# Kernel tuning notes

Measured on AMD Instinct MI355X. Metric: run time of the kernel, lower is better.

The kernel has to match this reference:

```python
import jax, jax.numpy as jnp
import numpy as np

N = 50000        # nodes
E = 800000       # edges
F_IN = 16        # num_features
F_EDGE = 8       # num_edge_features
H = 4            # heads
C = 32           # hidden_dim (per-head out channels)
D = H * C        # 128, node state width
NUM_CLASSES = 5
NEG_SLOPE = 0.2  # PyG GATConv default leaky_relu slope


def setup_inputs() -> dict:
    key = jax.random.key(0)
    ks = jax.random.split(key, 30)
    def w(k, shape):
        return jax.random.normal(k, shape, dtype=jnp.float32) * 0.05
    return {
        "x": jax.random.normal(ks[0], (N, F_IN), dtype=jnp.float32),
        "edge_index": jax.random.randint(ks[1], (2, E), 0, N),
        "edge_attr": jax.random.normal(ks[2], (E, F_EDGE), dtype=jnp.float32),
        # edge_encoder: Linear(F_EDGE->C), ReLU, Linear(C->H)
        "ee_w1": w(ks[3], (C, F_EDGE)), "ee_b1": jnp.zeros((C,), jnp.float32),
        "ee_w2": w(ks[4], (H, C)),      "ee_b2": jnp.zeros((H,), jnp.float32),
        # input_proj: Linear(F_IN -> D)
        "proj_w": w(ks[5], (D, F_IN)), "proj_b": jnp.zeros((D,), jnp.float32),
        # conv1: GATConv(F_IN, C, heads=H, edge_dim=H, concat=True)
        "c1_lin": w(ks[6], (D, F_IN)),
        "c1_att_src": w(ks[7], (H, C)), "c1_att_dst": w(ks[8], (H, C)),
        "c1_lin_edge": w(ks[9], (D, H)), "c1_att_edge": w(ks[10], (H, C)),
        "c1_bias": jnp.zeros((D,), jnp.float32),
        # conv2: GATConv(D, C, heads=H, edge_dim=H, concat=True)
        "c2_lin": w(ks[11], (D, D)),
        "c2_att_src": w(ks[12], (H, C)), "c2_att_dst": w(ks[13], (H, C)),
        "c2_lin_edge": w(ks[14], (D, H)), "c2_att_edge": w(ks[15], (H, C)),
        "c2_bias": jnp.zeros((D,), jnp.float32),
        # layer norms
        "n1_g": jnp.ones((D,), jnp.float32), "n1_b": jnp.zeros((D,), jnp.float32),
        "n2_g": jnp.ones((D,), jnp.float32), "n2_b": jnp.zeros((D,), jnp.float32),
        # jk_proj: Linear(3D -> D)
        "jk_w": w(ks[16], (D, 3 * D)), "jk_b": jnp.zeros((D,), jnp.float32),
        # classifier: Linear(D -> NUM_CLASSES)
        "cls_w": w(ks[17], (NUM_CLASSES, D)), "cls_b": jnp.zeros((NUM_CLASSES,), jnp.float32),
    }


def _layer_norm(h, g, b, eps=1e-5):
    mu = jnp.mean(h, axis=-1, keepdims=True)
    var = jnp.var(h, axis=-1, keepdims=True)
    return (h - mu) * jax.lax.rsqrt(var + eps) * g + b


def _gat_conv(x, src, dst, e_attr, lin_w, att_src, att_dst, lin_edge_w, att_edge, bias):
    """PyG GATConv (v1) with edge features, concat=True, eval mode (no dropout)."""
    n = x.shape[0]
    xs = (x @ lin_w.T).reshape(n, H, C)                      # [N,H,C]
    a_src = jnp.einsum('nhc,hc->nh', xs, att_src)            # [N,H]
    a_dst = jnp.einsum('nhc,hc->nh', xs, att_dst)            # [N,H]
    ee = (e_attr @ lin_edge_w.T).reshape(-1, H, C)           # [E,H,C]
    a_edge = jnp.einsum('ehc,hc->eh', ee, att_edge)          # [E,H]
    alpha = jax.nn.leaky_relu(a_src[src] + a_dst[dst] + a_edge, NEG_SLOPE)
    # segment softmax over destination neighborhoods
    amax = jax.ops.segment_max(alpha, dst, num_segments=n)
    ex = jnp.exp(alpha - amax[dst])
    denom = jax.ops.segment_sum(ex, dst, num_segments=n)
    alpha = ex / (denom[dst] + 1e-16)                        # [E,H]
    msg = xs[src] * alpha[:, :, None]                        # [E,H,C]
    out = jax.ops.segment_sum(msg, dst, num_segments=n)      # [N,H,C]
    return out.reshape(n, H * C) + bias


def reference(x, edge_index, edge_attr,
              ee_w1, ee_b1, ee_w2, ee_b2,
              proj_w, proj_b,
              c1_lin, c1_att_src, c1_att_dst, c1_lin_edge, c1_att_edge, c1_bias,
              c2_lin, c2_att_src, c2_att_dst, c2_lin_edge, c2_att_edge, c2_bias,
              n1_g, n1_b, n2_g, n2_b,
              jk_w, jk_b, cls_w, cls_b):
    src, dst = edge_index[0], edge_index[1]
    # edge encoder
    e = jax.nn.relu(edge_attr @ ee_w1.T + ee_b1) @ ee_w2.T + ee_b2   # [E,H]
    h0 = x @ proj_w.T + proj_b                                        # [N,D]
    h1 = _gat_conv(x, src, dst, e, c1_lin, c1_att_src, c1_att_dst,
                   c1_lin_edge, c1_att_edge, c1_bias)
    h1 = _layer_norm(jax.nn.elu(h1) + h0, n1_g, n1_b)
    h2 = _gat_conv(h1, src, dst, e, c2_lin, c2_att_src, c2_att_dst,
                   c2_lin_edge, c2_att_edge, c2_bias)
    h2 = _layer_norm(jax.nn.elu(h2) + h1, n2_g, n2_b)
    h = jnp.concatenate([h0, h1, h2], axis=-1) @ jk_w.T + jk_b
    out = h @ cls_w.T + cls_b
    return jax.nn.log_softmax(out, axis=1)
```

## Files before the change

kernel.cpp:

```cpp
#include <hip/hip_runtime.h>
#include <cstdint>

#define NN 50000
#define NE 800000
#define DPX 6250
#define SLICES 391

using short8  = __attribute__((ext_vector_type(8))) short;
using float4v = __attribute__((ext_vector_type(4))) float;
using floatx2 = __attribute__((ext_vector_type(2))) float;
typedef unsigned char uchar;

__device__ __forceinline__ ushort f2bf(float f) {
    uint u = __float_as_uint(f);
    uint r = (u + 0x7fffu + ((u >> 16) & 1u)) >> 16;
    return (ushort)r;
}
__device__ __forceinline__ float bf2f(uint u) {
    return __uint_as_float(u << 16);
}
__device__ __forceinline__ uchar f2fp8(float v) {
    return (uchar)((uint)__builtin_amdgcn_cvt_pk_fp8_f32(v, v, 0, false) & 0xffu);
}

__global__ __launch_bounds__(256) void k_prep2(const float* __restrict__ le1, const float* __restrict__ ae1,
                                               const float* __restrict__ le2, const float* __restrict__ ae2,
                                               const float* __restrict__ jkw, const float* __restrict__ jkb,
                                               const float* __restrict__ clw, const float* __restrict__ clb,
                                               const float* __restrict__ projw, const float* __restrict__ c1lin,
                                               const float* __restrict__ c2lin,
                                               const float* __restrict__ asrc1, const float* __restrict__ adst1,
                                               float* __restrict__ M, float* __restrict__ CW,
                                               float* __restrict__ cbp,
                                               ushort* __restrict__ w01b, ushort* __restrict__ c2b,
                                               float* __restrict__ Vmat, int* __restrict__ deg)
{
    int idx = blockIdx.x * 256 + threadIdx.x;
    if (idx < NN) deg[idx] = 0;
    if (idx < 32) {
        const float* le = (idx < 16) ? le1 : le2;
        const float* ae = (idx < 16) ? ae1 : ae2;
        int hk = idx & 15, h = hk >> 2, k = hk & 3;
        float s = 0.f;
        for (int c = 0; c < 32; ++c)
            s += le[(h * 32 + c) * 4 + k] * ae[h * 32 + c];
        M[idx] = s;
    } else if (idx < 1952) {
        int o = idx - 32;
        int r = o / 384, c = o - r * 384;
        float s = 0.f;
        for (int k = 0; k < 128; ++k)
            s += clw[r * 128 + k] * jkw[(size_t)k * 384 + c];
        CW[o] = s;
    } else if (idx < 1957) {
        int r = idx - 1952;
        float s = clb[r];
        for (int k = 0; k < 128; ++k)
            s += clw[r * 128 + k] * jkb[k];
        cbp[r] = s;
    } else if (idx >= 2048 && idx < 10240) {
        int o = idx - 2048;
        int r = o >> 5, c = o & 31;
        float v = 0.f;
        if (c < 16) v = (r < 128) ? projw[r * 16 + c] : c1lin[(r - 128) * 16 + c];
        w01b[o] = f2bf(v);
    } else if (idx >= 10240 && idx < 26624) {
        int o = idx - 10240;
        c2b[o] = f2bf(c2lin[o]);
    } else if (idx >= 26624 && idx < 26752) {
        int o = idx - 26624;
        const float* att = (o < 64) ? asrc1 : adst1;
        int oo = o & 63, h = oo >> 4, k = oo & 15;
        float s = 0.f;
        for (int c = 0; c < 32; ++c)
            s += c1lin[(h * 32 + c) * 16 + k] * att[h * 32 + c];
        Vmat[o] = s;
    }
}

__global__ __launch_bounds__(256) void k_att1(const float* __restrict__ x,
                                              const float* __restrict__ V,
                                              float* __restrict__ as_o,
                                              float* __restrict__ ad_o)
{
    __shared__ float sV[128];
    int t = threadIdx.x;
    if (t < 128) sV[t] = V[t];
    __syncthreads();
    int n = blockIdx.x * 256 + t;
    if (n >= NN) return;
    const float4* xr = (const float4*)(x + (size_t)n * 16);
    float4 x0 = xr[0], x1 = xr[1], x2 = xr[2], x3 = xr[3];
    float xv[16] = {x0.x,x0.y,x0.z,x0.w, x1.x,x1.y,x1.z,x1.w,
                    x2.x,x2.y,x2.z,x2.w, x3.x,x3.y,x3.z,x3.w};
    float s[4], d[4];
    #pragma unroll
    for (int h = 0; h < 4; ++h) {
        float ss = 0.f, dd = 0.f;
        #pragma unroll
        for (int k = 0; k < 16; ++k) {
            ss += xv[k] * sV[h * 16 + k];
            dd += xv[k] * sV[64 + h * 16 + k];
        }
        s[h] = ss; d[h] = dd;
    }
    *(float4*)(as_o + (size_t)n * 4) = make_float4(s[0], s[1], s[2], s[3]);
    *(float4*)(ad_o + (size_t)n * 4) = make_float4(d[0], d[1], d[2], d[3]);
}

__global__ __launch_bounds__(256) void k_edge_mlp(const float* __restrict__ ea,
                                                  const float* __restrict__ w1,
                                                  const float* __restrict__ b1,
                                                  const float* __restrict__ w2,
                                                  const float* __restrict__ b2,
                                                  const int* __restrict__ ei,
                                                  const float* __restrict__ Mm,
                                                  const float* __restrict__ as1,
                                                  const float* __restrict__ ad1,
                                                  ushort* __restrict__ exb,
                                                  uint* __restrict__ aeq)
{
    __shared__ float sw1[256], sb1[32], sw2[128], sb2[4], sM[32];
    int t = threadIdx.x;
    sw1[t] = w1[t];
    if (t < 128) sw2[t] = w2[t];
    if (t < 32)  { sb1[t] = b1[t]; sM[t] = Mm[t]; }
    if (t < 4)   sb2[t] = b2[t];
    __syncthreads();
    int e = blockIdx.x * 256 + t;
    if (e >= NE) return;
    int src = ei[e], dst = ei[NE + e];
    float4 s4 = *(const float4*)(as1 + (size_t)src * 4);
    float4 d4 = *(const float4*)(ad1 + (size_t)dst * 4);
    float4 x0 = *(const float4*)(ea + (size_t)e * 8);
    float4 x1 = *(const float4*)(ea + (size_t)e * 8 + 4);
    float o0 = sb2[0], o1 = sb2[1], o2 = sb2[2], o3 = sb2[3];
    #pragma unroll
    for (int j = 0; j < 32; ++j) {
        const float* w = sw1 + j * 8;
        float s = sb1[j] + w[0]*x0.x + w[1]*x0.y + w[2]*x0.z + w[3]*x0.w
                         + w[4]*x1.x + w[5]*x1.y + w[6]*x1.z + w[7]*x1.w;
        s = fmaxf(s, 0.f);
        o0 += sw2[0*32+j] * s; o1 += sw2[1*32+j] * s;
        o2 += sw2[2*32+j] * s; o3 += sw2[3*32+j] * s;
    }
    float sa[4] = {s4.x, s4.y, s4.z, s4.w};
    float da[4] = {d4.x, d4.y, d4.z, d4.w};
    ushort exq[4];
    float a2[4];
    #pragma unroll
    for (int h = 0; h < 4; ++h) {
        float ae1 = sM[h*4+0]*o0 + sM[h*4+1]*o1 + sM[h*4+2]*o2 + sM[h*4+3]*o3;
        float al = sa[h] + da[h] + ae1;
        al = al > 0.f ? al : 0.2f * al;
        exq[h] = f2bf(__expf(al));
        a2[h] = sM[16+h*4+0]*o0 + sM[16+h*4+1]*o1 + sM[16+h*4+2]*o2 + sM[16+h*4+3]*o3;
    }
    *(uint2*)(exb + (size_t)e * 4) =
        make_uint2((uint)exq[0] | ((uint)exq[1] << 16), (uint)exq[2] | ((uint)exq[3] << 16));
    uint q = (uint)__builtin_amdgcn_cvt_pk_fp8_f32(a2[0], a2[1], 0, false);
    q = (uint)__builtin_amdgcn_cvt_pk_fp8_f32(a2[2], a2[3], (int)q, true);
    aeq[e] = q;
}

__global__ __launch_bounds__(256) void k_hist8(const int* __restrict__ ei, int* __restrict__ deg)
{
    int grp = blockIdx.x & 7;
    int base = (blockIdx.x >> 3) * 2048 + threadIdx.x;
    #pragma unroll
    for (int k = 0; k < 8; ++k) {
        int e = base + k * 256;
        if (e < NE) {
            int dst = ei[NE + e];
            if (dst / DPX == grp) atomicAdd(&deg[dst], 1);
        }
    }
}

__global__ __launch_bounds__(256) void k_scan_blk(const int* __restrict__ deg,
                                                  int* __restrict__ loc,
                                                  int* __restrict__ bsum)
{
    __shared__ int tmp[256];
    int t = threadIdx.x;
    int i = blockIdx.x * 256 + t;
    int v = (i < NN) ? deg[i] : 0;
    tmp[t] = v;
    __syncthreads();
    #pragma unroll
    for (int o = 1; o < 256; o <<= 1) {
        int add = (t >= o) ? tmp[t - o] : 0;
        __syncthreads();
        tmp[t] += add;
        __syncthreads();
    }
    if (i < NN) loc[i] = tmp[t] - v;
    if (t == 255) bsum[blockIdx.x] = tmp[255];
}

__global__ __launch_bounds__(256) void k_scan_top(const int* __restrict__ bsum,
                                                  int* __restrict__ bcarry,
                                                  int* __restrict__ total_out, int nb)
{
    __shared__ int tmp[256];
    int t = threadIdx.x;
    int v = (t < nb) ? bsum[t] : 0;
    tmp[t] = v;
    __syncthreads();
    #pragma unroll
    for (int o = 1; o < 256; o <<= 1) {
        int add = (t >= o) ? tmp[t - o] : 0;
        __syncthreads();
        tmp[t] += add;
        __syncthreads();
    }
    if (t < nb) bcarry[t] = tmp[t] - v;
    if (t == 255) *total_out = tmp[255];
}

__global__ __launch_bounds__(256) void k_scan_add(const int* __restrict__ loc,
                                                  const int* __restrict__ bcarry,
                                                  int* __restrict__ off,
                                                  int* __restrict__ cur)
{
    int i = blockIdx.x * 256 + threadIdx.x;
    if (i < NN) {
        int o = loc[i] + bcarry[blockIdx.x];
        off[i] = o;
        cur[i] = o;
    }
}

__global__ __launch_bounds__(256) void k_scatter8(const int* __restrict__ ei,
                                                  const ushort* __restrict__ exb,
                                                  const uint* __restrict__ aeq,
                                                  int* __restrict__ cursor,
                                                  int4* __restrict__ csr4)
{
    int grp = blockIdx.x & 7;
    int base = (blockIdx.x >> 3) * 2048 + threadIdx.x;
    #pragma unroll
    for (int k = 0; k < 8; ++k) {
        int e = base + k * 256;
        if (e < NE) {
            int dst = ei[NE + e];
            if (dst / DPX == grp) {
                int src = ei[e];
                uint2 ex = *(const uint2*)(exb + (size_t)e * 4);
                uint q = aeq[e];
                int p = atomicAdd(&cursor[dst], 1);
                csr4[p] = make_int4((src << 16) | dst, (int)ex.x, (int)ex.y, (int)q);
            }
        }
    }
}

__global__ __launch_bounds__(256) void k_gemm1(const float* __restrict__ x,
                                               const ushort* __restrict__ w01,
                                               const float* __restrict__ pbias,
                                               ushort* __restrict__ hcatb,
                                               uchar* __restrict__ xs8, int M)
{
    int t = threadIdx.x;
    int wv = t >> 6, lane = t & 63;
    int quad = lane >> 4, r16 = lane & 15;
    int m0 = blockIdx.x * 128 + wv * 32;
    int ar0 = m0 + r16;      if (ar0 >= M) ar0 = M - 1;
    int ar1 = m0 + 16 + r16; if (ar1 >= M) ar1 = M - 1;
    short8 a0 = (short8){0,0,0,0,0,0,0,0}, a1 = a0;
    if (quad < 2) {
        const float* p0 = x + (size_t)ar0 * 16 + quad * 8;
        const float* p1 = x + (size_t)ar1 * 16 + quad * 8;
        float4 u0 = *(const float4*)p0, u1 = *(const float4*)(p0 + 4);
        float4 v0 = *(const float4*)p1, v1 = *(const float4*)(p1 + 4);
        a0[0]=(short)f2bf(u0.x); a0[1]=(short)f2bf(u0.y); a0[2]=(short)f2bf(u0.z); a0[3]=(short)f2bf(u0.w);
        a0[4]=(short)f2bf(u1.x); a0[5]=(short)f2bf(u1.y); a0[6]=(short)f2bf(u1.z); a0[7]=(short)f2bf(u1.w);
        a1[0]=(short)f2bf(v0.x); a1[1]=(short)f2bf(v0.y); a1[2]=(short)f2bf(v0.z); a1[3]=(short)f2bf(v0.w);
        a1[4]=(short)f2bf(v1.x); a1[5]=(short)f2bf(v1.y); a1[6]=(short)f2bf(v1.z); a1[7]=(short)f2bf(v1.w);
    }
    float4v acc[2][16];
    #pragma unroll
    for (int i = 0; i < 2; ++i)
        #pragma unroll
        for (int j = 0; j < 16; ++j) acc[i][j] = (float4v){0.f, 0.f, 0.f, 0.f};
    #pragma unroll
    for (int nt = 0; nt < 16; ++nt) {
        short8 b = *(const short8*)(w01 + (size_t)(nt * 16 + r16) * 32 + quad * 8);
        acc[0][nt] = __builtin_amdgcn_mfma_f32_16x16x32_bf16(a0, b, acc[0][nt], 0, 0, 0);
        acc[1][nt] = __builtin_amdgcn_mfma_f32_16x16x32_bf16(a1, b, acc[1][nt], 0, 0, 0);
    }
    #pragma unroll
    for (int rt = 0; rt < 2; ++rt) {
        #pragma unroll
        for (int nt = 0; nt < 16; ++nt) {
            int col = (nt & 7) * 16 + r16;
            float bv = (nt < 8) ? pbias[col] : 0.f;
            #pragma unroll
            for (int r = 0; r < 4; ++r) {
                int row = m0 + rt * 16 + quad * 4 + r;
                if (row < M) {
                    float v = acc[rt][nt][r] + bv;
                    if (nt < 8) hcatb[(size_t)row * 384 + col] = f2bf(v);
                    else        xs8[(size_t)row * 128 + col] = f2fp8(v);
                }
            }
        }
    }
}

__global__ __launch_bounds__(256) void k_gemm2(const ushort* __restrict__ A,
                                               const ushort* __restrict__ W,
                                               const float* __restrict__ atts,
                                               const float* __restrict__ attd,
                                               uchar* __restrict__ xs8,
                                               float* __restrict__ as_o,
                                               float* __restrict__ ad_o, int M)
{
    __shared__ float sAs[128], sAd[128];
    int t = threadIdx.x;
    if (t < 128) { sAs[t] = atts[t]; sAd[t] = attd[t]; }
    __syncthreads();
    int wv = t >> 6, lane = t & 63;
    int quad = lane >> 4, r16 = lane & 15;
    int m0 = blockIdx.x * 128 + wv * 32;
    float4v acc[2][8];
    #pragma unroll
    for (int i = 0; i < 2; ++i)
        #pragma unroll
        for (int j = 0; j < 8; ++j) acc[i][j] = (float4v){0.f, 0.f, 0.f, 0.f};
    int ar0 = m0 + r16;      if (ar0 >= M) ar0 = M - 1;
    int ar1 = m0 + 16 + r16; if (ar1 >= M) ar1 = M - 1;
    const ushort* a0p = A + (size_t)ar0 * 384 + quad * 8;
    const ushort* a1p = A + (size_t)ar1 * 384 + quad * 8;
    const ushort* wp  = W + (size_t)r16 * 128 + quad * 8;
    #pragma unroll
    for (int k0 = 0; k0 < 128; k0 += 32) {
        short8 a0 = *(const short8*)(a0p + k0);
        short8 a1 = *(const short8*)(a1p + k0);
        #pragma unroll
        for (int nt = 0; nt < 8; ++nt) {
            short8 b = *(const short8*)(wp + (size_t)(nt * 16) * 128 + k0);
            acc[0][nt] = __builtin_amdgcn_mfma_f32_16x16x32_bf16(a0, b, acc[0][nt], 0, 0, 0);
            acc[1][nt] = __builtin_amdgcn_mfma_f32_16x16x32_bf16(a1, b, acc[1][nt], 0, 0, 0);
        }
    }
    #pragma unroll
    for (int rt = 0; rt < 2; ++rt) {
        #pragma unroll
        for (int nt = 0; nt < 8; ++nt) {
            int col = nt * 16 + r16;
            #pragma unroll
            for (int r = 0; r < 4; ++r) {
                int row = m0 + rt * 16 + quad * 4 + r;
                if (row < M)
                    xs8[(size_t)row * 128 + col] = f2fp8(acc[rt][nt][r]);
            }
        }
        #pragma unroll
        for (int r = 0; r < 4; ++r) {
            int row = m0 + rt * 16 + quad * 4 + r;
            float sh[4], dh[4];
            #pragma unroll
            for (int h = 0; h < 4; ++h) {
                int cA = h * 32 + r16, cB = cA + 16;
                sh[h] = acc[rt][2*h][r] * sAs[cA] + acc[rt][2*h+1][r] * sAs[cB];
                dh[h] = acc[rt][2*h][r] * sAd[cA] + acc[rt][2*h+1][r] * sAd[cB];
            }
            #pragma unroll
            for (int o = 1; o < 16; o <<= 1) {
                #pragma unroll
                for (int h = 0; h < 4; ++h) {
                    sh[h] += __shfl_xor(sh[h], o, 64);
                    dh[h] += __shfl_xor(dh[h], o, 64);
                }
            }
            if (r16 == 0 && row < M) {
                *(float4*)(as_o + (size_t)row * 4) = make_float4(sh[0], sh[1], sh[2], sh[3]);
                *(float4*)(ad_o + (size_t)row * 4) = make_float4(dh[0], dh[1], dh[2], dh[3]);
            }
        }
    }
}

__global__ __launch_bounds__(256) void k_soft2csr(int4* __restrict__ csr4,
                                                  const float* __restrict__ as_in,
                                                  const float* __restrict__ ad_in)
{
    int i = blockIdx.x * 256 + threadIdx.x;
    if (i >= NE) return;
    int4 en = csr4[i];
    uint sd = (uint)en.x;
    int src = (int)(sd >> 16), dst = (int)(sd & 0xffffu);
    float4 s4 = *(const float4*)(as_in + (size_t)src * 4);
    float4 d4 = *(const float4*)(ad_in + (size_t)dst * 4);
    floatx2 a01 = __builtin_amdgcn_cvt_pk_f32_fp8(en.w, false);
    floatx2 a23 = __builtin_amdgcn_cvt_pk_f32_fp8(en.w, true);
    float av[4] = {a01.x, a01.y, a23.x, a23.y};
    float sa[4] = {s4.x, s4.y, s4.z, s4.w};
    float da[4] = {d4.x, d4.y, d4.z, d4.w};
    ushort exq[4];
    #pragma unroll
    for (int h = 0; h < 4; ++h) {
        float al = sa[h] + da[h] + av[h];
        al = al > 0.f ? al : 0.2f * al;
        exq[h] = f2bf(__expf(al));
    }
    en.y = (int)((uint)exq[0] | ((uint)exq[1] << 16));
    en.z = (int)((uint)exq[2] | ((uint)exq[3] << 16));
    csr4[i] = en;
}

__global__ __launch_bounds__(256) void k_agg2(const int* __restrict__ off,
                                              const int4* __restrict__ csr4,
                                              const uchar* __restrict__ xs8,
                                              const float* __restrict__ bias,
                                              const ushort* __restrict__ residb,
                                              const float* __restrict__ g,
                                              const float* __restrict__ bln,
                                              ushort* __restrict__ outb)
{
    int wave = threadIdx.x >> 6;
    int lane = threadIdx.x & 63;
    int n = blockIdx.x * 4 + wave;
    if (n >= NN) return;
    int i0 = off[n], i1 = off[n + 1];
    int c0 = lane * 2;
    int h = lane >> 4;
    int hsel = h >> 1, hsh = (h & 1) << 4;
    float a0 = 0.f, a1 = 0.f, den = 0.f;
    int i = i0;
    for (; i + 8 <= i1; i += 8) {
        int4 en[8];
        #pragma unroll
        for (int j = 0; j < 8; ++j) en[j] = csr4[i + j];
        ushort p[8];
        #pragma unroll
        for (int j = 0; j < 8; ++j)
            p[j] = *(const ushort*)(xs8 + (size_t)((uint)en[j].x >> 16) * 128 + c0);
        #pragma unroll
        for (int j = 0; j < 8; ++j) {
            uint exsel = (uint)(hsel ? en[j].z : en[j].y);
            float w = bf2f((exsel >> hsh) & 0xffffu);
            floatx2 v = __builtin_amdgcn_cvt_pk_f32_fp8((int)(uint)p[j], false);
            a0 = fmaf(v.x, w, a0);
            a1 = fmaf(v.y, w, a1);
            den += w;
        }
    }
    for (; i + 4 <= i1; i += 4) {
        int4 en[4];
        #pragma unroll
        for (int j = 0; j < 4; ++j) en[j] = csr4[i + j];
        ushort p[4];
        #pragma unroll
        for (int j = 0; j < 4; ++j)
            p[j] = *(const ushort*)(xs8 + (size_t)((uint)en[j].x >> 16) * 128 + c0);
        #pragma unroll
        for (int j = 0; j < 4; ++j) {
            uint exsel = (uint)(hsel ? en[j].z : en[j].y);
            float w = bf2f((exsel >> hsh) & 0xffffu);
            floatx2 v = __builtin_amdgcn_cvt_pk_f32_fp8((int)(uint)p[j], false);
            a0 = fmaf(v.x, w, a0);
            a1 = fmaf(v.y, w, a1);
            den += w;
        }
    }
    for (; i < i1; ++i) {
        int4 en = csr4[i];
        ushort p0 = *(const ushort*)(xs8 + (size_t)((uint)en.x >> 16) * 128 + c0);
        uint exsel = (uint)(hsel ? en.z : en.y);
        float w = bf2f((exsel >> hsh) & 0xffffu);
        floatx2 v = __builtin_amdgcn_cvt_pk_f32_fp8((int)(uint)p0, false);
        a0 = fmaf(v.x, w, a0);
        a1 = fmaf(v.y, w, a1);
        den += w;
    }
    float inv = 1.f / (den + 1e-16f);
    float v0 = a0 * inv + bias[c0];
    float v1 = a1 * inv + bias[c0 + 1];
    v0 = v0 > 0.f ? v0 : (__expf(v0) - 1.f);
    v1 = v1 > 0.f ? v1 : (__expf(v1) - 1.f);
    uint rp = *(const uint*)(residb + (size_t)n * 384 + c0);
    float r0 = v0 + bf2f(rp & 0xffffu);
    float r1 = v1 + bf2f(rp >> 16);
    float ssum = r0 + r1, ssq = r0 * r0 + r1 * r1;
    #pragma unroll
    for (int o = 1; o < 64; o <<= 1) {
        ssum += __shfl_xor(ssum, o, 64);
        ssq  += __shfl_xor(ssq, o, 64);
    }
    float mu = ssum * (1.f / 128.f);
    float var = ssq * (1.f / 128.f) - mu * mu;
    float rs = rsqrtf(var + 1e-5f);
    float o0 = (r0 - mu) * rs * g[c0] + bln[c0];
    float o1 = (r1 - mu) * rs * g[c0 + 1] + bln[c0 + 1];
    uint pk = (uint)f2bf(o0) | ((uint)f2bf(o1) << 16);
    *(uint*)(outb + (size_t)n * 384 + c0) = pk;
}

__global__ __launch_bounds__(256) void k_cls(const ushort* __restrict__ hcatb,
                                             const float* __restrict__ CW,
                                             const float* __restrict__ cbp,
                                             float* __restrict__ out)
{
    __shared__ float sCW[1920], scb[5];
    int t = threadIdx.x;
    for (int i = t; i < 1920; i += 256) sCW[i] = CW[i];
    if (t < 5) scb[t] = cbp[t];
    __syncthreads();
    int n = blockIdx.x * 256 + t;
    if (n >= NN) return;
    float acc[5] = {scb[0], scb[1], scb[2], scb[3], scb[4]};
    const uint2* hr = (const uint2*)(hcatb + (size_t)n * 384);
    #pragma unroll 4
    for (int q = 0; q < 96; ++q) {
        uint2 p = hr[q];
        float v0 = bf2f(p.x & 0xffffu), v1 = bf2f(p.x >> 16);
        float v2 = bf2f(p.y & 0xffffu), v3 = bf2f(p.y >> 16);
        #pragma unroll
        for (int o = 0; o < 5; ++o) {
            const float* w = sCW + o * 384 + q * 4;
            acc[o] += v0*w[0] + v1*w[1] + v2*w[2] + v3*w[3];
        }
    }
    float m = acc[0];
    #pragma unroll
    for (int o = 1; o < 5; ++o) m = fmaxf(m, acc[o]);
    float sum = 0.f;
    #pragma unroll
    for (int o = 0; o < 5; ++o) sum += __expf(acc[o] - m);
    float lse = __logf(sum) + m;
    float* op = out + (size_t)n * 5;
    #pragma unroll
    for (int o = 0; o < 5; ++o) op[o] = acc[o] - lse;
}

extern "C" void kernel_launch(void* const* d_in, const int* in_sizes, int n_in,
                              void* d_out, int out_size, void* d_ws, size_t ws_size,
                              hipStream_t stream)
{
    (void)in_sizes; (void)n_in; (void)out_size; (void)ws_size;
    const float* x        = (const float*)d_in[0];
    const int*   ei       = (const int*)d_in[1];
    const float* eattr    = (const float*)d_in[2];
    const float* ee_w1    = (const float*)d_in[3];
    const float* ee_b1    = (const float*)d_in[4];
    const float* ee_w2    = (const float*)d_in[5];
    const float* ee_b2    = (const float*)d_in[6];
    const float* proj_w   = (const float*)d_in[7];
    const float* proj_b   = (const float*)d_in[8];
    const float* c1_lin   = (const float*)d_in[9];
    const float* c1_asrc  = (const float*)d_in[10];
    const float* c1_adst  = (const float*)d_in[11];
    const float* c1_ledge = (const float*)d_in[12];
    const float* c1_aedge = (const float*)d_in[13];
    const float* c1_bias  = (const float*)d_in[14];
    const float* c2_lin   = (const float*)d_in[15];
    const float* c2_asrc  = (const float*)d_in[16];
    const float* c2_adst  = (const float*)d_in[17];
    const float* c2_ledge = (const float*)d_in[18];
    const float* c2_aedge = (const float*)d_in[19];
    const float* c2_bias  = (const float*)d_in[20];
    const float* n1_g     = (const float*)d_in[21];
    const float* n1_b     = (const float*)d_in[22];
    const float* n2_g     = (const float*)d_in[23];
    const float* n2_b     = (const float*)d_in[24];
    const float* jk_w     = (const float*)d_in[25];
    const float* jk_b     = (const float*)d_in[26];
    const float* cls_w    = (const float*)d_in[27];
    const float* cls_b    = (const float*)d_in[28];
    float* out = (float*)d_out;
    float* ws  = (float*)d_ws;

    const size_t oM   = 0;
    const size_t oCW  = 64;
    const size_t oCB  = 1984;
    const size_t oV   = 2048;
    const size_t oEX  = 2176;
    const size_t oAQ  = oEX + (size_t)NE * 2;
    const size_t oHB  = oAQ + (size_t)NE;
    const size_t oXS  = oHB + (size_t)NN * 192;
    const size_t oWB  = oXS + (size_t)NN * 32;
    const size_t oAS  = oWB + 12288;
    const size_t oAD  = oAS + (size_t)NN * 4;
    const size_t oI   = oAD + (size_t)NN * 4;

    float*  Mmat  = ws + oM;
    float*  CW    = ws + oCW;
    float*  cbp   = ws + oCB;
    float*  Vmat  = ws + oV;
    ushort* exb   = (ushort*)(ws + oEX);
    uint*   aeq   = (uint*)(ws + oAQ);
    ushort* hcatb = (ushort*)(ws + oHB);
    uchar*  xs8   = (uchar*)(ws + oXS);
    ushort* w01b  = (ushort*)(ws + oWB);
    ushort* c2b   = w01b + 8192;
    float*  as_b  = ws + oAS;
    float*  ad_b  = ws + oAD;
    int*    ip    = (int*)(ws + oI);
    int*    deg   = ip;
    int*    loc   = ip + NN;
    int*    off   = ip + 2 * NN;
    int*    cur   = ip + 3 * NN + 16;
    int*    bsum  = ip + 4 * NN + 16;
    int*    bcar  = ip + 4 * NN + 272;
    int4*   csr4  = (int4*)(ip + 4 * NN + 544);

    const int EB  = (NE + 255) / 256;
    const int NB  = (NN + 255) / 256;
    const int GB  = (NN + 127) / 128;
    const int WB2 = (NN + 3) / 4;
    const int PB  = SLICES * 8;

    k_prep2<<<NB, 256, 0, stream>>>(c1_ledge, c1_aedge, c2_ledge, c2_aedge,
                                    jk_w, jk_b, cls_w, cls_b,
                                    proj_w, c1_lin, c2_lin, c1_asrc, c1_adst,
                                    Mmat, CW, cbp, w01b, c2b, Vmat, deg);
    k_att1<<<NB, 256, 0, stream>>>(x, Vmat, as_b, ad_b);
    k_edge_mlp<<<EB, 256, 0, stream>>>(eattr, ee_w1, ee_b1, ee_w2, ee_b2, ei,
                                       Mmat, as_b, ad_b, exb, aeq);
    k_hist8<<<PB, 256, 0, stream>>>(ei, deg);
    k_scan_blk<<<NB, 256, 0, stream>>>(deg, loc, bsum);
    k_scan_top<<<1, 256, 0, stream>>>(bsum, bcar, off + NN, NB);
    k_scan_add<<<NB, 256, 0, stream>>>(loc, bcar, off, cur);
    k_scatter8<<<PB, 256, 0, stream>>>(ei, exb, aeq, cur, csr4);

    k_gemm1<<<GB, 256, 0, stream>>>(x, w01b, proj_b, hcatb, xs8, NN);

    k_agg2<<<WB2, 256, 0, stream>>>(off, csr4, xs8, c1_bias, hcatb,
                                    n1_g, n1_b, hcatb + 128);

    k_gemm2<<<GB, 256, 0, stream>>>(hcatb + 128, c2b, c2_asrc, c2_adst,
                                    xs8, as_b, ad_b, NN);
    k_soft2csr<<<EB, 256, 0, stream>>>(csr4, as_b, ad_b);
    k_agg2<<<WB2, 256, 0, stream>>>(off, csr4, xs8, c2_bias, hcatb + 128,
                                    n2_g, n2_b, hcatb + 256);

    k_cls<<<NB, 256, 0, stream>>>(hcatb, CW, cbp, out);
}
```

Measured before the change: 380.7 us.

## Defer layer-1 softmax to CSR pass, pack edge records, split aggregation across two waves

The edge MLP now writes a packed int4 record (src/dst, bf16 layer-1 edge logits, fp8 layer-2 logits) so the scatter copies one record instead of gathering three arrays. The layer-1 attention source/destination scores are computed inside gemm1 from its accumulators, which removes the separate k_att1 kernel and the V-matrix prep. The exp for layer 1 moves into a new k_soft1csr pass over CSR order. The aggregation kernel now gives each node two waves that take alternating edges and combine their partial sums through shared memory, which raises parallelism on the gather. The cost is an extra full-edge pass, a block-wide sync in aggregation, and a launch of NN/2 blocks that assumes NN is even.

```diff
diff --git a/kernel.cpp b/kernel.cpp
--- a/kernel.cpp
+++ b/kernel.cpp
@@ -29,11 +29,10 @@
                                                const float* __restrict__ clw, const float* __restrict__ clb,
                                                const float* __restrict__ projw, const float* __restrict__ c1lin,
                                                const float* __restrict__ c2lin,
-                                               const float* __restrict__ asrc1, const float* __restrict__ adst1,
                                                float* __restrict__ M, float* __restrict__ CW,
                                                float* __restrict__ cbp,
                                                ushort* __restrict__ w01b, ushort* __restrict__ c2b,
-                                               float* __restrict__ Vmat, int* __restrict__ deg)
+                                               int* __restrict__ deg)
 {
     int idx = blockIdx.x * 256 + threadIdx.x;
     if (idx < NN) deg[idx] = 0;
@@ -67,45 +66,7 @@
     } else if (idx >= 10240 && idx < 26624) {
         int o = idx - 10240;
         c2b[o] = f2bf(c2lin[o]);
-    } else if (idx >= 26624 && idx < 26752) {
-        int o = idx - 26624;
-        const float* att = (o < 64) ? asrc1 : adst1;
-        int oo = o & 63, h = oo >> 4, k = oo & 15;
-        float s = 0.f;
-        for (int c = 0; c < 32; ++c)
-            s += c1lin[(h * 32 + c) * 16 + k] * att[h * 32 + c];
-        Vmat[o] = s;
-    }
-}
-
-__global__ __launch_bounds__(256) void k_att1(const float* __restrict__ x,
-                                              const float* __restrict__ V,
-                                              float* __restrict__ as_o,
-                                              float* __restrict__ ad_o)
-{
-    __shared__ float sV[128];
-    int t = threadIdx.x;
-    if (t < 128) sV[t] = V[t];
-    __syncthreads();
-    int n = blockIdx.x * 256 + t;
-    if (n >= NN) return;
-    const float4* xr = (const float4*)(x + (size_t)n * 16);
-    float4 x0 = xr[0], x1 = xr[1], x2 = xr[2], x3 = xr[3];
-    float xv[16] = {x0.x,x0.y,x0.z,x0.w, x1.x,x1.y,x1.z,x1.w,
-                    x2.x,x2.y,x2.z,x2.w, x3.x,x3.y,x3.z,x3.w};
-    float s[4], d[4];
-    #pragma unroll
-    for (int h = 0; h < 4; ++h) {
-        float ss = 0.f, dd = 0.f;
-        #pragma unroll
-        for (int k = 0; k < 16; ++k) {
-            ss += xv[k] * sV[h * 16 + k];
-            dd += xv[k] * sV[64 + h * 16 + k];
-        }
-        s[h] = ss; d[h] = dd;
-    }
-    *(float4*)(as_o + (size_t)n * 4) = make_float4(s[0], s[1], s[2], s[3]);
-    *(float4*)(ad_o + (size_t)n * 4) = make_float4(d[0], d[1], d[2], d[3]);
+    }
 }
 
 __global__ __launch_bounds__(256) void k_edge_mlp(const float* __restrict__ ea,
@@ -115,10 +76,7 @@
                                                   const float* __restrict__ b2,
                                                   const int* __restrict__ ei,
                                                   const float* __restrict__ Mm,
-                                                  const float* __restrict__ as1,
-                                                  const float* __restrict__ ad1,
-                                                  ushort* __restrict__ exb,
-                                                  uint* __restrict__ aeq)
+                                                  int4* __restrict__ rec)
 {
     __shared__ float sw1[256], sb1[32], sw2[128], sb2[4], sM[32];
     int t = threadIdx.x;
@@ -130,8 +88,6 @@
     int e = blockIdx.x * 256 + t;
     if (e >= NE) return;
     int src = ei[e], dst = ei[NE + e];
-    float4 s4 = *(const float4*)(as1 + (size_t)src * 4);
-    float4 d4 = *(const float4*)(ad1 + (size_t)dst * 4);
     float4 x0 = *(const float4*)(ea + (size_t)e * 8);
     float4 x1 = *(const float4*)(ea + (size_t)e * 8 + 4);
     float o0 = sb2[0], o1 = sb2[1], o2 = sb2[2], o3 = sb2[3];
@@ -144,23 +100,19 @@
         o0 += sw2[0*32+j] * s; o1 += sw2[1*32+j] * s;
         o2 += sw2[2*32+j] * s; o3 += sw2[3*32+j] * s;
     }
-    float sa[4] = {s4.x, s4.y, s4.z, s4.w};
-    float da[4] = {d4.x, d4.y, d4.z, d4.w};
-    ushort exq[4];
+    ushort a1q[4];
     float a2[4];
     #pragma unroll
     for (int h = 0; h < 4; ++h) {
-        float ae1 = sM[h*4+0]*o0 + sM[h*4+1]*o1 + sM[h*4+2]*o2 + sM[h*4+3]*o3;
-        float al = sa[h] + da[h] + ae1;
-        al = al > 0.f ? al : 0.2f * al;
-        exq[h] = f2bf(__expf(al));
-        a2[h] = sM[16+h*4+0]*o0 + sM[16+h*4+1]*o1 + sM[16+h*4+2]*o2 + sM[16+h*4+3]*o3;
-    }
-    *(uint2*)(exb + (size_t)e * 4) =
-        make_uint2((uint)exq[0] | ((uint)exq[1] << 16), (uint)exq[2] | ((uint)exq[3] << 16));
+        a1q[h] = f2bf(sM[h*4+0]*o0 + sM[h*4+1]*o1 + sM[h*4+2]*o2 + sM[h*4+3]*o3);
+        a2[h]  = sM[16+h*4+0]*o0 + sM[16+h*4+1]*o1 + sM[16+h*4+2]*o2 + sM[16+h*4+3]*o3;
+    }
     uint q = (uint)__builtin_amdgcn_cvt_pk_fp8_f32(a2[0], a2[1], 0, false);
     q = (uint)__builtin_amdgcn_cvt_pk_fp8_f32(a2[2], a2[3], (int)q, true);
-    aeq[e] = q;
+    rec[e] = make_int4((src << 16) | dst,
+                       (int)((uint)a1q[0] | ((uint)a1q[1] << 16)),
+                       (int)((uint)a1q[2] | ((uint)a1q[3] << 16)),
+                       (int)q);
 }
 
 __global__ __launch_bounds__(256) void k_hist8(const int* __restrict__ ei, int* __restrict__ deg)
@@ -231,9 +183,7 @@
     }
 }
 
-__global__ __launch_bounds__(256) void k_scatter8(const int* __restrict__ ei,
-                                                  const ushort* __restrict__ exb,
-                                                  const uint* __restrict__ aeq,
+__global__ __launch_bounds__(256) void k_scatter8(const int4* __restrict__ rec,
                                                   int* __restrict__ cursor,
                                                   int4* __restrict__ csr4)
 {
@@ -243,25 +193,85 @@
     for (int k = 0; k < 8; ++k) {
         int e = base + k * 256;
         if (e < NE) {
-            int dst = ei[NE + e];
+            int4 r = rec[e];
+            int dst = r.x & 0xffff;
             if (dst / DPX == grp) {
-                int src = ei[e];
-                uint2 ex = *(const uint2*)(exb + (size_t)e * 4);
-                uint q = aeq[e];
                 int p = atomicAdd(&cursor[dst], 1);
-                csr4[p] = make_int4((src << 16) | dst, (int)ex.x, (int)ex.y, (int)q);
-            }
-        }
-    }
+                csr4[p] = r;
+            }
+        }
+    }
+}
+
+__global__ __launch_bounds__(256) void k_soft1csr(int4* __restrict__ csr4,
+                                                  const float* __restrict__ as_in,
+                                                  const float* __restrict__ ad_in)
+{
+    int i = blockIdx.x * 256 + threadIdx.x;
+    if (i >= NE) return;
+    int4 en = csr4[i];
+    uint sd = (uint)en.x;
+    int src = (int)(sd >> 16), dst = (int)(sd & 0xffffu);
+    float4 s4 = *(const float4*)(as_in + (size_t)src * 4);
+    float4 d4 = *(const float4*)(ad_in + (size_t)dst * 4);
+    float av[4] = {bf2f((uint)en.y & 0xffffu), bf2f((uint)en.y >> 16),
+                   bf2f((uint)en.z & 0xffffu), bf2f((uint)en.z >> 16)};
+    float sa[4] = {s4.x, s4.y, s4.z, s4.w};
+    float da[4] = {d4.x, d4.y, d4.z, d4.w};
+    ushort exq[4];
+    #pragma unroll
+    for (int h = 0; h < 4; ++h) {
+        float al = sa[h] + da[h] + av[h];
+        al = al > 0.f ? al : 0.2f * al;
+        exq[h] = f2bf(__expf(al));
+    }
+    en.y = (int)((uint)exq[0] | ((uint)exq[1] << 16));
+    en.z = (int)((uint)exq[2] | ((uint)exq[3] << 16));
+    csr4[i] = en;
+}
+
+__global__ __launch_bounds__(256) void k_soft2csr(int4* __restrict__ csr4,
+                                                  const float* __restrict__ as_in,
+                                                  const float* __restrict__ ad_in)
+{
+    int i = blockIdx.x * 256 + threadIdx.x;
+    if (i >= NE) return;
+    int4 en = csr4[i];
+    uint sd = (uint)en.x;
+    int src = (int)(sd >> 16), dst = (int)(sd & 0xffffu);
+    float4 s4 = *(const float4*)(as_in + (size_t)src * 4);
+    float4 d4 = *(const float4*)(ad_in + (size_t)dst * 4);
+    floatx2 a01 = __builtin_amdgcn_cvt_pk_f32_fp8(en.w, false);
+    floatx2 a23 = __builtin_amdgcn_cvt_pk_f32_fp8(en.w, true);
+    float av[4] = {a01.x, a01.y, a23.x, a23.y};
+    float sa[4] = {s4.x, s4.y, s4.z, s4.w};
+    float da[4] = {d4.x, d4.y, d4.z, d4.w};
+    ushort exq[4];
+    #pragma unroll
+    for (int h = 0; h < 4; ++h) {
+        float al = sa[h] + da[h] + av[h];
+        al = al > 0.f ? al : 0.2f * al;
+        exq[h] = f2bf(__expf(al));
+    }
+    en.y = (int)((uint)exq[0] | ((uint)exq[1] << 16));
+    en.z = (int)((uint)exq[2] | ((uint)exq[3] << 16));
+    csr4[i] = en;
 }
 
 __global__ __launch_bounds__(256) void k_gemm1(const float* __restrict__ x,
                                                const ushort* __restrict__ w01,
                                                const float* __restrict__ pbias,
+                                               const float* __restrict__ atts,
+                                               const float* __restrict__ attd,
                                                ushort* __restrict__ hcatb,
-                                               uchar* __restrict__ xs8, int M)
-{
+                                               uchar* __restrict__ xs8,
+                                               float* __restrict__ as_o,
+                                               float* __restrict__ ad_o, int M)
+{
+    __shared__ float sAs[128], sAd[128];
     int t = threadIdx.x;
+    if (t < 128) { sAs[t] = atts[t]; sAd[t] = attd[t]; }
+    __syncthreads();
     int wv = t >> 6, lane = t & 63;
     int quad = lane >> 4, r16 = lane & 15;
     int m0 = blockIdx.x * 128 + wv * 32;
@@ -305,6 +315,29 @@
                 }
             }
         }
+        #pragma unroll
+        for (int r = 0; r < 4; ++r) {
+            int row = m0 + rt * 16 + quad * 4 + r;
+            float sh[4], dh[4];
+            #pragma unroll
+            for (int h = 0; h < 4; ++h) {
+                int cA = h * 32 + r16, cB = cA + 16;
+                sh[h] = acc[rt][8+2*h][r] * sAs[cA] + acc[rt][8+2*h+1][r] * sAs[cB];
+                dh[h] = acc[rt][8+2*h][r] * sAd[cA] + acc[rt][8+2*h+1][r] * sAd[cB];
+            }
+            #pragma unroll
+            for (int o = 1; o < 16; o <<= 1) {
+                #pragma unroll
+                for (int h = 0; h < 4; ++h) {
+                    sh[h] += __shfl_xor(sh[h], o, 64);
+                    dh[h] += __shfl_xor(dh[h], o, 64);
+                }
+            }
+            if (r16 == 0 && row < M) {
+                *(float4*)(as_o + (size_t)row * 4) = make_float4(sh[0], sh[1], sh[2], sh[3]);
+                *(float4*)(ad_o + (size_t)row * 4) = make_float4(dh[0], dh[1], dh[2], dh[3]);
+            }
+        }
     }
 }
 
@@ -382,34 +415,6 @@
     }
 }
 
-__global__ __launch_bounds__(256) void k_soft2csr(int4* __restrict__ csr4,
-                                                  const float* __restrict__ as_in,
-                                                  const float* __restrict__ ad_in)
-{
-    int i = blockIdx.x * 256 + threadIdx.x;
-    if (i >= NE) return;
-    int4 en = csr4[i];
-    uint sd = (uint)en.x;
-    int src = (int)(sd >> 16), dst = (int)(sd & 0xffffu);
-    float4 s4 = *(const float4*)(as_in + (size_t)src * 4);
-    float4 d4 = *(const float4*)(ad_in + (size_t)dst * 4);
-    floatx2 a01 = __builtin_amdgcn_cvt_pk_f32_fp8(en.w, false);
-    floatx2 a23 = __builtin_amdgcn_cvt_pk_f32_fp8(en.w, true);
-    float av[4] = {a01.x, a01.y, a23.x, a23.y};
-    float sa[4] = {s4.x, s4.y, s4.z, s4.w};
-    float da[4] = {d4.x, d4.y, d4.z, d4.w};
-    ushort exq[4];
-    #pragma unroll
-    for (int h = 0; h < 4; ++h) {
-        float al = sa[h] + da[h] + av[h];
-        al = al > 0.f ? al : 0.2f * al;
-        exq[h] = f2bf(__expf(al));
-    }
-    en.y = (int)((uint)exq[0] | ((uint)exq[1] << 16));
-    en.z = (int)((uint)exq[2] | ((uint)exq[3] << 16));
-    csr4[i] = en;
-}
-
 __global__ __launch_bounds__(256) void k_agg2(const int* __restrict__ off,
                                               const int4* __restrict__ csr4,
                                               const uchar* __restrict__ xs8,
@@ -419,62 +424,56 @@
                                               const float* __restrict__ bln,
                                               ushort* __restrict__ outb)
 {
-    int wave = threadIdx.x >> 6;
-    int lane = threadIdx.x & 63;
-    int n = blockIdx.x * 4 + wave;
-    if (n >= NN) return;
+    __shared__ float comb[2][3][64];
+    int t = threadIdx.x;
+    int wv = t >> 6, lane = t & 63;
+    int ns = wv >> 1, j = wv & 1;
+    int n = blockIdx.x * 2 + ns;
     int i0 = off[n], i1 = off[n + 1];
     int c0 = lane * 2;
     int h = lane >> 4;
     int hsel = h >> 1, hsh = (h & 1) << 4;
     float a0 = 0.f, a1 = 0.f, den = 0.f;
-    int i = i0;
-    for (; i + 8 <= i1; i += 8) {
-        int4 en[8];
-        #pragma unroll
-        for (int j = 0; j < 8; ++j) en[j] = csr4[i + j];
-        ushort p[8];
-        #pragma unroll
-        for (int j = 0; j < 8; ++j)
-            p[j] = *(const ushort*)(xs8 + (size_t)((uint)en[j].x >> 16) * 128 + c0);
-        #pragma unroll
-        for (int j = 0; j < 8; ++j) {
-            uint exsel = (uint)(hsel ? en[j].z : en[j].y);
-            float w = bf2f((exsel >> hsh) & 0xffffu);
-            floatx2 v = __builtin_amdgcn_cvt_pk_f32_fp8((int)(uint)p[j], false);
-            a0 = fmaf(v.x, w, a0);
-            a1 = fmaf(v.y, w, a1);
-            den += w;
-        }
-    }
-    for (; i + 4 <= i1; i += 4) {
-        int4 en[4];
-        #pragma unroll
-        for (int j = 0; j < 4; ++j) en[j] = csr4[i + j];
-        ushort p[4];
-        #pragma unroll
-        for (int j = 0; j < 4; ++j)
-            p[j] = *(const ushort*)(xs8 + (size_t)((uint)en[j].x >> 16) * 128 + c0);
-        #pragma unroll
-        for (int j = 0; j < 4; ++j) {
-            uint exsel = (uint)(hsel ? en[j].z : en[j].y);
-            float w = bf2f((exsel >> hsh) & 0xffffu);
-            floatx2 v = __builtin_amdgcn_cvt_pk_f32_fp8((int)(uint)p[j], false);
-            a0 = fmaf(v.x, w, a0);
-            a1 = fmaf(v.y, w, a1);
-            den += w;
-        }
-    }
-    for (; i < i1; ++i) {
-        int4 en = csr4[i];
-        ushort p0 = *(const ushort*)(xs8 + (size_t)((uint)en.x >> 16) * 128 + c0);
-        uint exsel = (uint)(hsel ? en.z : en.y);
-        float w = bf2f((exsel >> hsh) & 0xffffu);
-        floatx2 v = __builtin_amdgcn_cvt_pk_f32_fp8((int)(uint)p0, false);
-        a0 = fmaf(v.x, w, a0);
-        a1 = fmaf(v.y, w, a1);
-        den += w;
-    }
+    int i = i0 + j;
+    for (; i + 6 < i1; i += 8) {
+        int4 e0 = csr4[i], e1 = csr4[i+2], e2 = csr4[i+4], e3 = csr4[i+6];
+        ushort p0 = *(const ushort*)(xs8 + (size_t)((uint)e0.x >> 16) * 128 + c0);
+        ushort p1 = *(const ushort*)(xs8 + (size_t)((uint)e1.x >> 16) * 128 + c0);
+        ushort p2 = *(const ushort*)(xs8 + (size_t)((uint)e2.x >> 16) * 128 + c0);
+        ushort p3 = *(const ushort*)(xs8 + (size_t)((uint)e3.x >> 16) * 128 + c0);
+        float w0 = bf2f(((uint)(hsel ? e0.z : e0.y) >> hsh) & 0xffffu);
+        float w1 = bf2f(((uint)(hsel ? e1.z : e1.y) >> hsh) & 0xffffu);
+        float w2 = bf2f(((uint)(hsel ? e2.z : e2.y) >> hsh) & 0xffffu);
+        float w3 = bf2f(((uint)(hsel ? e3.z : e3.y) >> hsh) & 0xffffu);
+        floatx2 v0 = __builtin_amdgcn_cvt_pk_f32_fp8((int)(uint)p0, false);
+        floatx2 v1 = __builtin_amdgcn_cvt_pk_f32_fp8((int)(uint)p1, false);
+        floatx2 v2 = __builtin_amdgcn_cvt_pk_f32_fp8((int)(uint)p2, false);
+        floatx2 v3 = __builtin_amdgcn_cvt_pk_f32_fp8((int)(uint)p3, false);
+        a0 = fmaf(v0.x, w0, a0); a1 = fmaf(v0.y, w0, a1);
+        a0 = fmaf(v1.x, w1, a0); a1 = fmaf(v1.y, w1, a1);
+        a0 = fmaf(v2.x, w2, a0); a1 = fmaf(v2.y, w2, a1);
+        a0 = fmaf(v3.x, w3, a0); a1 = fmaf(v3.y, w3, a1);
+        den += (w0 + w1) + (w2 + w3);
+    }
+    for (; i < i1; i += 2) {
+        int4 e0 = csr4[i];
+        ushort p0 = *(const ushort*)(xs8 + (size_t)((uint)e0.x >> 16) * 128 + c0);
+        float w0 = bf2f(((uint)(hsel ? e0.z : e0.y) >> hsh) & 0xffffu);
+        floatx2 v0 = __builtin_amdgcn_cvt_pk_f32_fp8((int)(uint)p0, false);
+        a0 = fmaf(v0.x, w0, a0);
+        a1 = fmaf(v0.y, w0, a1);
+        den += w0;
+    }
+    if (j == 1) {
+        comb[ns][0][lane] = a0;
+        comb[ns][1][lane] = a1;
+        comb[ns][2][lane] = den;
+    }
+    __syncthreads();
+    if (j == 1) return;
+    a0 += comb[ns][0][lane];
+    a1 += comb[ns][1][lane];
+    den += comb[ns][2][lane];
     float inv = 1.f / (den + 1e-16f);
     float v0 = a0 * inv + bias[c0];
     float v1 = a1 * inv + bias[c0 + 1];
@@ -575,10 +574,8 @@
     const size_t oM   = 0;
     const size_t oCW  = 64;
     const size_t oCB  = 1984;
-    const size_t oV   = 2048;
-    const size_t oEX  = 2176;
-    const size_t oAQ  = oEX + (size_t)NE * 2;
-    const size_t oHB  = oAQ + (size_t)NE;
+    const size_t oREC = 2048;
+    const size_t oHB  = oREC + (size_t)NE * 4;
     const size_t oXS  = oHB + (size_t)NN * 192;
     const size_t oWB  = oXS + (size_t)NN * 32;
     const size_t oAS  = oWB + 12288;
@@ -588,9 +585,7 @@
     float*  Mmat  = ws + oM;
     float*  CW    = ws + oCW;
     float*  cbp   = ws + oCB;
-    float*  Vmat  = ws + oV;
-    ushort* exb   = (ushort*)(ws + oEX);
-    uint*   aeq   = (uint*)(ws + oAQ);
+    int4*   rec   = (int4*)(ws + oREC);
     ushort* hcatb = (ushort*)(ws + oHB);
     uchar*  xs8   = (uchar*)(ws + oXS);
     ushort* w01b  = (ushort*)(ws + oWB);
@@ -609,31 +604,31 @@
     const int EB  = (NE + 255) / 256;
     const int NB  = (NN + 255) / 256;
     const int GB  = (NN + 127) / 128;
-    const int WB2 = (NN + 3) / 4;
+    const int AGB = NN / 2;
     const int PB  = SLICES * 8;
 
     k_prep2<<<NB, 256, 0, stream>>>(c1_ledge, c1_aedge, c2_ledge, c2_aedge,
                                     jk_w, jk_b, cls_w, cls_b,
-                                    proj_w, c1_lin, c2_lin, c1_asrc, c1_adst,
-                                    Mmat, CW, cbp, w01b, c2b, Vmat, deg);
-    k_att1<<<NB, 256, 0, stream>>>(x, Vmat, as_b, ad_b);
-    k_edge_mlp<<<EB, 256, 0, stream>>>(eattr, ee_w1, ee_b1, ee_w2, ee_b2, ei,
-                                       Mmat, as_b, ad_b, exb, aeq);
+                                    proj_w, c1_lin, c2_lin,
+                                    Mmat, CW, cbp, w01b, c2b, deg);
+    k_edge_mlp<<<EB, 256, 0, stream>>>(eattr, ee_w1, ee_b1, ee_w2, ee_b2, ei, Mmat, rec);
     k_hist8<<<PB, 256, 0, stream>>>(ei, deg);
     k_scan_blk<<<NB, 256, 0, stream>>>(deg, loc, bsum);
     k_scan_top<<<1, 256, 0, stream>>>(bsum, bcar, off + NN, NB);
     k_scan_add<<<NB, 256, 0, stream>>>(loc, bcar, off, cur);
-    k_scatter8<<<PB, 256, 0, stream>>>(ei, exb, aeq, cur, csr4);
-
-    k_gemm1<<<GB, 256, 0, stream>>>(x, w01b, proj_b, hcatb, xs8, NN);
-
-    k_agg2<<<WB2, 256, 0, stream>>>(off, csr4, xs8, c1_bias, hcatb,
+    k_scatter8<<<PB, 256, 0, stream>>>(rec, cur, csr4);
+
+    k_gemm1<<<GB, 256, 0, stream>>>(x, w01b, proj_b, c1_asrc, c1_adst,
+                                    hcatb, xs8, as_b, ad_b, NN);
+
+    k_soft1csr<<<EB, 256, 0, stream>>>(csr4, as_b, ad_b);
+    k_agg2<<<AGB, 256, 0, stream>>>(off, csr4, xs8, c1_bias, hcatb,
                                     n1_g, n1_b, hcatb + 128);
 
     k_gemm2<<<GB, 256, 0, stream>>>(hcatb + 128, c2b, c2_asrc, c2_adst,
                                     xs8, as_b, ad_b, NN);
     k_soft2csr<<<EB, 256, 0, stream>>>(csr4, as_b, ad_b);
-    k_agg2<<<WB2, 256, 0, stream>>>(off, csr4, xs8, c2_bias, hcatb + 128,
+    k_agg2<<<AGB, 256, 0, stream>>>(off, csr4, xs8, c2_bias, hcatb + 128,
                                     n2_g, n2_b, hcatb + 256);
 
     k_cls<<<NB, 256, 0, stream>>>(hcatb, CW, cbp, out);
```

Result: slower. 414.9 us (+9.0%).
